# Performance work log

Measured on AMD Instinct MI355X. Metric: run time of the kernel, lower is better.

Reference implementation:

```python
import jax, jax.numpy as jnp
import numpy as np

HEADS = 5

def _conv2d(x, w, b=None, groups=1):
    y = jax.lax.conv_general_dilated(x, w, (1, 1), 'SAME', feature_group_count=groups,
                                     dimension_numbers=('NCHW', 'OIHW', 'NCHW'))
    return y if b is None else y + b[None, :, None, None]

def _conv1d(x, w):
    return jax.lax.conv_general_dilated(x, w, (1,), [(2, 2)], dimension_numbers=('NCH', 'OIH', 'NCH'))

def _bn(x, g, b, eps=1e-5):
    # torch BatchNorm2d in training mode: biased batch stats over (N,H,W)
    m = jnp.mean(x, (0, 2, 3), keepdims=True)
    v = jnp.var(x, (0, 2, 3), keepdims=True)
    return g[None, :, None, None] * (x - m) * jax.lax.rsqrt(v + eps) + b[None, :, None, None]

def _avg_pool3s2(x):
    # AvgPool2d(3, stride=2, padding=1), count_include_pad=True -> divide by 9
    s = jax.lax.reduce_window(x, 0.0, jax.lax.add, (1, 1, 3, 3), (1, 1, 2, 2),
                              [(0, 0), (0, 0), (1, 1), (1, 1)])
    return s / 9.0

def _max_pool2(x):
    return jax.lax.reduce_window(x, -jnp.inf, jax.lax.max, (1, 1, 2, 2), (1, 1, 2, 2), [(0, 0)] * 4)

def _gauss_kernel(ks, sigma, ch):
    # replicates cv2.getGaussianKernel(ks, sigma) outer-product, depthwise weight (ch,1,ks,ks)
    i = np.arange(ks, dtype=np.float64) - (ks - 1) / 2.0
    g = np.exp(-(i ** 2) / (2.0 * sigma ** 2))
    g = g / g.sum()
    k2 = np.outer(g, g).astype(np.float32)
    return jnp.asarray(np.broadcast_to(k2, (ch, 1, ks, ks)).copy())

def _forward(x, dwconv_w, dwconv_b, qkvl_w, qkvl_b, reproj_w, reproj_b, queries_w, queries_b,
             sff_low_w, sff_low_g, sff_low_b, sff_high_w, sff_high_g, sff_high_b,
             sff_c1_w, sff_c2_w, out_conv_w, out_bn_g, out_bn_b, out_proj_w, out_proj_b):
    n, C, h, w = x.shape
    C4 = C // 4
    shortcut = x
    # local branch: channel-split, depthwise conv / pointwise qkvl
    x1 = jax.nn.gelu(_conv2d(x[:, ::2], dwconv_w, dwconv_b, groups=C // 2), approximate=False)
    x2 = jax.nn.gelu(_conv2d(x[:, 1::2], qkvl_w, qkvl_b), approximate=False)
    x2 = x2.reshape(n, HEADS, C4, h, w)
    q = jnp.sum(x2[:, :-3], axis=1)              # (n, C4, h, w)
    k = x2[:, -3]
    q = _avg_pool3s2(q).reshape(n, C4, -1)       # h,w even -> same pooled size, pad branch dead
    k = _max_pool2(k).reshape(n, C4, -1)
    v = x2[:, -2].reshape(n, C4, h * w)
    lfeat = x2[:, -1]
    qk = jnp.einsum('ncp,ndp->ncd', q, k)        # (n, cq, ck)
    A = jax.nn.softmax(qk, axis=1)               # softmax over cq, transpose folded into einsum
    x2o = jnp.einsum('nqk,nqp->nkp', A, v).reshape(n, C4, h, w)
    eff = _conv2d(jnp.concatenate([x1, lfeat, x2o], axis=1), reproj_w, reproj_b)
    # global frequency (Laplacian pyramid) channel attention
    qx = _conv2d(x, queries_w, queries_b).reshape(n, -1, C)
    q_ = jnp.transpose(jax.nn.softmax(qx, axis=1), (0, 2, 1))    # (n, C, hw)
    sigma0, s = 1.6, 2.0 ** (1.0 / 3.0)
    G = shortcut
    pyr = [G]
    for i in range(3):
        G = _conv2d(G, _gauss_kernel(2 * i + 3, sigma0 * s ** i, C), groups=C)
        pyr.append(G)
    ctx = ((pyr[0] - pyr[1]) + (pyr[1] - pyr[2]) + (pyr[2] - pyr[3])).reshape(n, C, h * w)
    att = jnp.einsum('ncp,ndp->ncd', jax.nn.softmax(ctx, axis=2), ctx)   # (n, C, C)
    freq = x + jnp.einsum('nji,njp->nip', att, q_).reshape(n, C, h, w)   # att.T @ q_
    # SFF fusion
    x_low = jax.nn.relu(_bn(_conv2d(freq, sff_low_w), sff_low_g, sff_low_b))
    x_high = jax.nn.relu(_bn(_conv2d(eff, sff_high_w), sff_high_g, sff_high_b))
    pl = (jnp.mean(x_low ** 3.0, axis=(2, 3)) + 1e-12) ** (1.0 / 3.0)    # GeM p=3 -> (n, C)
    ph = (jnp.mean(x_high ** 3.0, axis=(2, 3)) + 1e-12) ** (1.0 / 3.0)
    d = jnp.stack([pl, ph], axis=2).reshape(n, 1, 2 * C)                 # interleave low/high per channel
    d = _conv1d(_conv1d(d, sff_c1_w), sff_c2_w)
    d = jax.nn.sigmoid(d.reshape(n, C, 2))
    f = d[:, :, 0][:, :, None, None] * x_low + d[:, :, 1][:, :, None, None] * x_high
    # BiSeNetOutput head (PixelShuffle(1) is identity)
    y = jax.nn.relu(_bn(_conv2d(f, out_conv_w), out_bn_g, out_bn_b))
    return _conv2d(y, out_proj_w, out_proj_b)

def _w(k, shape):
    fan_in = int(np.prod(shape[1:]))
    return jax.random.normal(k, shape, jnp.float32) / np.sqrt(fan_in)

def setup_inputs() -> dict:
    keys = jax.random.split(jax.random.key(0), 12)
    C = 128
    f32 = jnp.float32
    return {
        'x': jax.random.normal(keys[0], (8, C, 128, 128), f32),
        'dwconv_w': _w(keys[1], (C // 2, 1, 3, 3)), 'dwconv_b': jnp.zeros((C // 2,), f32),
        'qkvl_w': _w(keys[2], (C // 4 * HEADS, C // 2, 1, 1)), 'qkvl_b': jnp.zeros((C // 4 * HEADS,), f32),
        'reproj_w': _w(keys[3], (C, C, 1, 1)), 'reproj_b': jnp.zeros((C,), f32),
        'queries_w': _w(keys[4], (C, C, 1, 1)), 'queries_b': jnp.zeros((C,), f32),
        'sff_low_w': _w(keys[5], (C, C, 3, 3)), 'sff_low_g': jnp.ones((C,), f32), 'sff_low_b': jnp.zeros((C,), f32),
        'sff_high_w': _w(keys[6], (C, C, 3, 3)), 'sff_high_g': jnp.ones((C,), f32), 'sff_high_b': jnp.zeros((C,), f32),
        'sff_c1_w': _w(keys[7], (1, 1, 5)), 'sff_c2_w': _w(keys[8], (1, 1, 5)),
        'out_conv_w': _w(keys[9], (C, C, 3, 3)), 'out_bn_g': jnp.ones((C,), f32), 'out_bn_b': jnp.zeros((C,), f32),
        'out_proj_w': _w(keys[10], (C, C, 1, 1)), 'out_proj_b': jnp.zeros((C,), f32),
    }

def reference(x, dwconv_w, dwconv_b, qkvl_w, qkvl_b, reproj_w, reproj_b, queries_w, queries_b,
              sff_low_w, sff_low_g, sff_low_b, sff_high_w, sff_high_g, sff_high_b,
              sff_c1_w, sff_c2_w, out_conv_w, out_bn_g, out_bn_b, out_proj_w, out_proj_b):
    return _forward(x, dwconv_w, dwconv_b, qkvl_w, qkvl_b, reproj_w, reproj_b, queries_w, queries_b,
                    sff_low_w, sff_low_g, sff_low_b, sff_high_w, sff_high_g, sff_high_b,
                    sff_c1_w, sff_c2_w, out_conv_w, out_bn_g, out_bn_b, out_proj_w, out_proj_b)
```

## Files before the change

kernel.cpp:

```cpp
#include <hip/hip_runtime.h>
#include <hip/hip_bf16.h>
#include <cmath>

#define DEVFN __device__ __forceinline__

constexpr int HW = 16384;
constexpr long long U = 16777216LL;
constexpr long long NHWC_N = 2163200LL;

typedef __attribute__((ext_vector_type(8))) short bf16x8;
typedef __attribute__((ext_vector_type(4))) float f32x4;
typedef __attribute__((ext_vector_type(4))) unsigned short u16x4;

constexpr long long OFF_X1   = 0;
constexpr long long OFF_QS   = U/2;
constexpr long long OFF_KK   = 3*U/4;
constexpr long long OFF_X2O  = U/2;
constexpr long long OFF_V    = U;
constexpr long long OFF_LF   = U + U/4;
constexpr long long OFF_QP   = U + U/2;
constexpr long long OFF_KP   = U + U/2 + 1048576;
constexpr long long S0       = 2*U;
constexpr long long OFF_QKB  = S0;
constexpr long long OFF_AA   = S0 + 8192;
constexpr long long OFF_MQ   = S0 + 16384;
constexpr long long OFF_DQ   = S0 + 17408;
constexpr long long OFF_PMAX = S0 + 18432;
constexpr long long OFF_PSUM = S0 + 149504;
constexpr long long OFF_MC   = S0 + 280576;
constexpr long long OFF_DC   = S0 + 281600;
constexpr long long OFF_ATT  = S0 + 282624;
constexpr long long OFF_SSL  = S0 + 430080;
constexpr long long OFF_SSH  = S0 + 430336;
constexpr long long OFF_SSY  = S0 + 430592;
constexpr long long OFF_DV   = S0 + 430848;
constexpr long long OFF_D0   = S0 + 432896;
constexpr long long OFF_D1   = S0 + 433920;
constexpr long long OFF_WQK  = S0 + 434944;
constexpr long long OFF_WLOW  = OFF_PMAX;
constexpr long long OFF_WHIGH = OFF_PMAX + 73728;
constexpr long long OFF_WOUT  = OFF_PMAX + 147456;
constexpr long long DOFF_CTXP  = 9000000;
constexpr long long DOFF_PARTA = 9100000;
constexpr long long DOFF_PARTB = 9700000;

struct Taps { float g[7]; };

DEVFN float gelu_f(float v) { return 0.5f * v * (1.0f + erff(v * 0.7071067811865475f)); }
DEVFN unsigned short f2b(float f) {
  unsigned u = __float_as_uint(f);
  unsigned r = u + 0x7fffu + ((u >> 16) & 1u);
  return (unsigned short)(r >> 16);
}
DEVFN unsigned pk2(float a, float b) {
  return (unsigned)f2b(a) | ((unsigned)f2b(b) << 16);
}

__global__ __launch_bounds__(256) void k_dwconv(const float* __restrict__ x, const float* __restrict__ w9,
                                                const float* __restrict__ bia, float* __restrict__ out) {
  int g = blockIdx.x * 256 + threadIdx.x;
  int w = g & 127, h = (g >> 7) & 127, c = (g >> 14) & 63, n = g >> 20;
  const float* src = x + (long long)(n * 128 + 2 * c) * HW;
  float acc = bia[c];
  #pragma unroll
  for (int ky = 0; ky < 3; ++ky) {
    int h2 = h + ky - 1;
    if ((unsigned)h2 < 128u) {
      #pragma unroll
      for (int kx = 0; kx < 3; ++kx) {
        int w2 = w + kx - 1;
        if ((unsigned)w2 < 128u) acc = fmaf(w9[c * 9 + ky * 3 + kx], src[h2 * 128 + w2], acc);
      }
    }
  }
  out[(long long)(n * 64 + c) * HW + h * 128 + w] = gelu_f(acc);
}

__global__ __launch_bounds__(256) void k_wpackq(const float* __restrict__ w, unsigned short* __restrict__ wp) {
  int g = blockIdx.x * 256 + threadIdx.x;
  if (g < 10240) wp[g] = f2b(w[g]);
}

__global__ __launch_bounds__(256) void k_qkvlm(const float* __restrict__ x, const unsigned short* __restrict__ wqk,
                                               const float* __restrict__ bq, float* __restrict__ qs,
                                               float* __restrict__ kk, float* __restrict__ vv,
                                               float* __restrict__ lf) {
  __shared__ unsigned int Bs[64 * 36];
  const int t = threadIdx.x;
  const int bx = blockIdx.x, n = blockIdx.y;
  const int pxb = bx * 64;
  #pragma unroll
  for (int it = 0; it < 8; ++it) {
    int e = it * 256 + t;
    int px = e & 63, k2 = e >> 6;
    float v0 = x[(long long)(n * 128 + 4 * k2 + 1) * HW + pxb + px];
    float v1 = x[(long long)(n * 128 + 4 * k2 + 3) * HW + pxb + px];
    Bs[px * 36 + k2] = pk2(v0, v1);
  }
  __syncthreads();
  const int wid = t >> 6, lane = t & 63, l15 = lane & 15, l4 = lane >> 4;
  f32x4 acc[10];
  #pragma unroll
  for (int m = 0; m < 10; ++m) { f32x4 z = {0.f,0.f,0.f,0.f}; acc[m] = z; }
  #pragma unroll
  for (int ks = 0; ks < 2; ++ks) {
    bf16x8 bfr = *(const bf16x8*)(&Bs[(wid * 16 + l15) * 36 + ks * 16 + l4 * 4]);
    #pragma unroll
    for (int mf = 0; mf < 10; ++mf) {
      bf16x8 af = *(const bf16x8*)(wqk + (mf * 16 + l15) * 64 + ks * 32 + l4 * 8);
      acc[mf] = __builtin_amdgcn_mfma_f32_16x16x32_bf16(af, bfr, acc[mf], 0, 0, 0);
    }
  }
  float* sT = (float*)Bs;
  const int pxl = wid * 16 + l15;
  const int jo = t >> 3, p0 = (t & 7) * 8;
  #pragma unroll
  for (int tau = 0; tau < 4; ++tau) {
    __syncthreads();
    #pragma unroll
    for (int mf = 0; mf < 2; ++mf) {
      #pragma unroll
      for (int r = 0; r < 4; ++r) {
        int j = mf * 16 + l4 * 4 + r;
        float v;
        if (tau == 0)
          v = gelu_f(acc[mf][r] + bq[j]) + gelu_f(acc[mf + 2][r] + bq[32 + j]);
        else
          v = gelu_f(acc[2 + 2 * tau + mf][r] + bq[32 * (tau + 1) + j]);
        sT[j * 68 + pxl] = v;
      }
    }
    __syncthreads();
    float* dstp = (tau == 0) ? qs : (tau == 1) ? kk : (tau == 2) ? vv : lf;
    long long o = (long long)(n * 32 + jo) * HW + pxb + p0;
    #pragma unroll
    for (int q4 = 0; q4 < 2; ++q4)
      *(f32x4*)&dstp[o + q4 * 4] = *(const f32x4*)&sT[jo * 68 + p0 + q4 * 4];
  }
}

__global__ __launch_bounds__(256) void k_avgpool(const float* __restrict__ in, float* __restrict__ out) {
  int g = blockIdx.x * 256 + threadIdx.x;
  int ow = g & 63, oh = (g >> 6) & 63, c = (g >> 12) & 31, n = g >> 17;
  const float* src = in + (long long)(n * 32 + c) * HW;
  float s = 0.f;
  #pragma unroll
  for (int i = 0; i < 3; ++i) {
    int h = oh * 2 - 1 + i;
    if ((unsigned)h < 128u) {
      #pragma unroll
      for (int j = 0; j < 3; ++j) {
        int w = ow * 2 - 1 + j;
        if ((unsigned)w < 128u) s += src[h * 128 + w];
      }
    }
  }
  out[(long long)(n * 32 + c) * 4096 + oh * 64 + ow] = s * (1.f / 9.f);
}

__global__ __launch_bounds__(256) void k_maxpool(const float* __restrict__ in, float* __restrict__ out) {
  int g = blockIdx.x * 256 + threadIdx.x;
  int ow = g & 63, oh = (g >> 6) & 63, c = (g >> 12) & 31, n = g >> 17;
  const float* src = in + (long long)(n * 32 + c) * HW;
  float m = -3.0e38f;
  #pragma unroll
  for (int i = 0; i < 2; ++i)
    #pragma unroll
    for (int j = 0; j < 2; ++j)
      m = fmaxf(m, src[(oh * 2 + i) * 128 + ow * 2 + j]);
  out[(long long)(n * 32 + c) * 4096 + oh * 64 + ow] = m;
}

__global__ __launch_bounds__(256) void k_qk(const float* __restrict__ qp, const float* __restrict__ kp,
                                            float* __restrict__ qk) {
  int c = blockIdx.x, n = blockIdx.y;
  int t = threadIdx.x, d = t >> 3, r = t & 7;
  const float* qr = qp + (long long)(n * 32 + c) * 4096;
  const float* kr = kp + (long long)(n * 32 + d) * 4096;
  float acc = 0.f;
  for (int p = r; p < 4096; p += 8) acc = fmaf(qr[p], kr[p], acc);
  acc += __shfl_down(acc, 4, 8);
  acc += __shfl_down(acc, 2, 8);
  acc += __shfl_down(acc, 1, 8);
  if (r == 0) qk[(n * 32 + c) * 32 + d] = acc;
}

__global__ void k_qksm(const float* __restrict__ qk, float* __restrict__ A) {
  int n = blockIdx.x, d = threadIdx.x;
  float m = -3.0e38f;
  for (int c = 0; c < 32; ++c) m = fmaxf(m, qk[(n * 32 + c) * 32 + d]);
  float s = 0.f;
  for (int c = 0; c < 32; ++c) s += expf(qk[(n * 32 + c) * 32 + d] - m);
  float inv = 1.f / s;
  for (int c = 0; c < 32; ++c) A[(n * 32 + c) * 32 + d] = expf(qk[(n * 32 + c) * 32 + d] - m) * inv;
}

__global__ __launch_bounds__(256) void k_x2o(const float* __restrict__ A, const float* __restrict__ vsrc,
                                             float* __restrict__ out) {
  __shared__ float lA[1024];
  int t = threadIdx.x;
  int g = blockIdx.x * 256 + t;
  int n = g >> 14, p = g & 16383;
  for (int e = t; e < 1024; e += 256) lA[e] = A[n * 1024 + e];
  __syncthreads();
  float acc[32];
  #pragma unroll
  for (int i = 0; i < 32; ++i) acc[i] = 0.f;
  for (int q = 0; q < 32; ++q) {
    float vv = vsrc[(long long)(n * 32 + q) * HW + p];
    #pragma unroll
    for (int k2 = 0; k2 < 32; ++k2) acc[k2] = fmaf(lA[q * 32 + k2], vv, acc[k2]);
  }
  #pragma unroll
  for (int k2 = 0; k2 < 32; ++k2) out[(long long)(n * 32 + k2) * HW + p] = acc[k2];
}

enum { M_EFF = 0, M_QX = 1, M_OUT = 2, M_FREQ = 3 };

template <int MODE>
__global__ __launch_bounds__(256) void k_gemm1x1m(
    const float* __restrict__ Amat, const float* __restrict__ B0, const float* __restrict__ B1,
    const float* __restrict__ B2, const float* __restrict__ bias, const float* __restrict__ scale,
    const float* __restrict__ Mq, const float* __restrict__ invDq, const float* __restrict__ xres,
    void* __restrict__ outp) {
  __shared__ unsigned int As[128 * 36];
  __shared__ unsigned int Bs[128 * 36];
  const int t = threadIdx.x;
  const int bx = blockIdx.x, n = blockIdx.y;
  const int pxb = bx * 128;
  const int wid = t >> 6, lane = t & 63, l15 = lane & 15, l4 = lane >> 4;
  const int wy = wid >> 1, wx = wid & 1;
  f32x4 acc[4][4];
  #pragma unroll
  for (int i = 0; i < 4; ++i)
    #pragma unroll
    for (int j = 0; j < 4; ++j) { f32x4 z = {0.f,0.f,0.f,0.f}; acc[i][j] = z; }

  for (int kc = 0; kc < 2; ++kc) {
    __syncthreads();
    if (MODE == M_FREQ) {
      #pragma unroll
      for (int it = 0; it < 16; ++it) {
        int e = it * 256 + t;
        int i = e & 127, j2l = e >> 7;
        int j = kc * 64 + 2 * j2l;
        float v0 = Amat[(long long)(n * 128 + j) * 128 + i];
        float v1 = Amat[(long long)(n * 128 + j + 1) * 128 + i];
        As[i * 36 + j2l] = pk2(v0, v1);
      }
    } else {
      #pragma unroll
      for (int it = 0; it < 16; ++it) {
        int e = it * 256 + t;
        int m = e >> 5, k2l = e & 31;
        float2 v = *(const float2*)(&Amat[m * 128 + kc * 64 + 2 * k2l]);
        As[m * 36 + k2l] = pk2(v.x, v.y);
      }
    }
    if (MODE == M_FREQ) {
      #pragma unroll
      for (int it = 0; it < 16; ++it) {
        int e = it * 256 + t;
        int j2l = e & 31, px = e >> 5;
        int j = kc * 64 + 2 * j2l;
        long long qb = ((long long)n * HW + pxb + px) * 128 + j;
        float2 v = *(const float2*)(&B0[qb]);
        float e0 = expf(v.x - Mq[n * 128 + j]) * invDq[n * 128 + j];
        float e1 = expf(v.y - Mq[n * 128 + j + 1]) * invDq[n * 128 + j + 1];
        Bs[px * 36 + j2l] = pk2(e0, e1);
      }
    } else {
      #pragma unroll
      for (int it = 0; it < 16; ++it) {
        int e = it * 256 + t;
        int px = e & 127, k2l = e >> 7;
        int ci = kc * 64 + 2 * k2l;
        float v0, v1;
        if (MODE == M_EFF) {
          if (ci < 64) {
            v0 = B0[(long long)(n * 64 + ci) * HW + pxb + px];
            v1 = B0[(long long)(n * 64 + ci + 1) * HW + pxb + px];
          } else if (ci < 96) {
            v0 = B1[(long long)(n * 32 + ci - 64) * HW + pxb + px];
            v1 = B1[(long long)(n * 32 + ci - 63) * HW + pxb + px];
          } else {
            v0 = B2[(long long)(n * 32 + ci - 96) * HW + pxb + px];
            v1 = B2[(long long)(n * 32 + ci - 95) * HW + pxb + px];
          }
        } else if (MODE == M_QX) {
          v0 = B0[(long long)(n * 128 + ci) * HW + pxb + px];
          v1 = B0[(long long)(n * 128 + ci + 1) * HW + pxb + px];
        } else {
          float u0 = B0[(long long)(n * 128 + ci) * HW + pxb + px];
          float u1 = B0[(long long)(n * 128 + ci + 1) * HW + pxb + px];
          v0 = fmaxf(fmaf(u0, scale[ci], scale[128 + ci]), 0.f);
          v1 = fmaxf(fmaf(u1, scale[ci + 1], scale[128 + ci + 1]), 0.f);
        }
        Bs[px * 36 + k2l] = pk2(v0, v1);
      }
    }
    __syncthreads();
    #pragma unroll
    for (int ks = 0; ks < 2; ++ks) {
      bf16x8 af[4], bfr[4];
      #pragma unroll
      for (int mf = 0; mf < 4; ++mf)
        af[mf] = *(const bf16x8*)(&As[(wy * 64 + mf * 16 + l15) * 36 + ks * 16 + l4 * 4]);
      #pragma unroll
      for (int nf = 0; nf < 4; ++nf)
        bfr[nf] = *(const bf16x8*)(&Bs[(wx * 64 + nf * 16 + l15) * 36 + ks * 16 + l4 * 4]);
      #pragma unroll
      for (int mf = 0; mf < 4; ++mf)
        #pragma unroll
        for (int nf = 0; nf < 4; ++nf)
          acc[mf][nf] = __builtin_amdgcn_mfma_f32_16x16x32_bf16(af[mf], bfr[nf], acc[mf][nf], 0, 0, 0);
    }
  }
  if (MODE == M_EFF || MODE == M_FREQ) {
    unsigned short* oT = (unsigned short*)outp;
    #pragma unroll
    for (int nf = 0; nf < 4; ++nf) {
      int px = pxb + wx * 64 + nf * 16 + l15;
      int hh = px >> 7, wwp = (px & 127) + 1;
      long long rb = (long long)n * NHWC_N + ((long long)(hh + 1) * 130 + wwp) * 128;
      #pragma unroll
      for (int mf = 0; mf < 4; ++mf) {
        int ch = wy * 64 + mf * 16 + l4 * 4;
        u16x4 pk;
        #pragma unroll
        for (int r = 0; r < 4; ++r) {
          float v = acc[mf][nf][r] + ((MODE == M_EFF) ? bias[ch + r] : 0.f);
          if (MODE == M_FREQ) v += xres[(long long)(n * 128 + ch + r) * HW + px];
          pk[r] = f2b(v);
        }
        *(u16x4*)(&oT[rb + ch]) = pk;
      }
    }
  } else {
    float* of = (float*)outp;
    #pragma unroll
    for (int mf = 0; mf < 4; ++mf)
      #pragma unroll
      for (int nf = 0; nf < 4; ++nf) {
        int px = pxb + wx * 64 + nf * 16 + l15;
        #pragma unroll
        for (int r = 0; r < 4; ++r) {
          int ch = wy * 64 + mf * 16 + l4 * 4 + r;
          of[(long long)(n * 128 + ch) * HW + px] = acc[mf][nf][r] + bias[ch];
        }
      }
  }
}

__global__ __launch_bounds__(128) void k_qx_stat1(const float* __restrict__ qx, float* __restrict__ pm,
                                                  float* __restrict__ ps) {
  int c = blockIdx.x, n = blockIdx.y, w = threadIdx.x;
  long long base = (long long)(n * 128 + c) * HW + w;
  float m = -3.0e38f;
  for (int h = 0; h < 128; ++h) m = fmaxf(m, qx[base + h * 128]);
  float s = 0.f;
  for (int h = 0; h < 128; ++h) s += expf(qx[base + h * 128] - m);
  pm[(n * 128 + c) * 128 + w] = m;
  ps[(n * 128 + c) * 128 + w] = s;
}
__global__ __launch_bounds__(128) void k_qx_stat2(const float* __restrict__ pm, const float* __restrict__ ps,
                                                  float* __restrict__ Mq, float* __restrict__ Dq) {
  int n = blockIdx.x, w = threadIdx.x;
  float M = -3.0e38f;
  for (int c = 0; c < 128; ++c) M = fmaxf(M, pm[(n * 128 + c) * 128 + w]);
  float D = 0.f;
  for (int c = 0; c < 128; ++c) D += ps[(n * 128 + c) * 128 + w] * expf(pm[(n * 128 + c) * 128 + w] - M);
  Mq[n * 128 + w] = M;
  Dq[n * 128 + w] = 1.f / D;
}

constexpr int BROWS = 44;
constexpr int BSTR  = 144;

template <int R, int HLO, int HHI, int VLO, int VHI>
DEVFN void blur_stage4(float* sA, float* sB, const float* __restrict__ g, int h0, int t) {
  __syncthreads();
  constexpr int HN = (HHI - HLO + 1) * 32;
  for (int e = t; e < HN; e += 256) {
    int r = HLO + (e >> 5), g4 = e & 31;
    int base = r * BSTR + 8 + g4 * 4;
    f32x4 a = *(const f32x4*)&sA[base - 4];
    f32x4 b = *(const f32x4*)&sA[base];
    f32x4 c = *(const f32x4*)&sA[base + 4];
    float m[12] = {a[0], a[1], a[2], a[3], b[0], b[1], b[2], b[3], c[0], c[1], c[2], c[3]};
    f32x4 s;
    #pragma unroll
    for (int j = 0; j < 4; ++j) {
      float acc = 0.f;
      #pragma unroll
      for (int d = -R; d <= R; ++d) acc = fmaf(g[d + R], m[4 + j + d], acc);
      s[j] = acc;
    }
    *(f32x4*)&sB[base] = s;
  }
  __syncthreads();
  constexpr int VN = (VHI - VLO + 1) * 32;
  for (int e = t; e < VN; e += 256) {
    int r = VLO + (e >> 5), g4 = e & 31;
    int base = r * BSTR + 8 + g4 * 4;
    f32x4 s = {0.f, 0.f, 0.f, 0.f};
    #pragma unroll
    for (int d = -R; d <= R; ++d) {
      f32x4 v = *(const f32x4*)&sB[base + d * BSTR];
      #pragma unroll
      for (int j = 0; j < 4; ++j) s[j] = fmaf(g[d + R], v[j], s[j]);
    }
    int h = h0 - 6 + r;
    if ((unsigned)h >= 128u) { f32x4 z = {0.f, 0.f, 0.f, 0.f}; s = z; }
    *(f32x4*)&sA[base] = s;
  }
}

__global__ __launch_bounds__(256) void k_blur3(const float* __restrict__ x, float* __restrict__ ctx,
                                               float* __restrict__ ctxp, Taps t3, Taps t5, Taps t7) {
  __shared__ float sA[BROWS * BSTR];
  __shared__ float sB[BROWS * BSTR];
  __shared__ float rm[256], rs[256];
  const int t = threadIdx.x;
  const int ht = blockIdx.x, h0 = ht * 32;
  const long long nc = blockIdx.y;
  const float* src = x + nc * HW;
  for (int e = t; e < BROWS * BSTR; e += 256) {
    int r = e / BSTR, wp = e % BSTR;
    int w = wp - 8, h = h0 - 6 + r;
    sA[e] = ((unsigned)h < 128u && (unsigned)w < 128u) ? src[h * 128 + w] : 0.f;
  }
  blur_stage4<1, 0, 43, 1, 42>(sA, sB, t3.g, h0, t);
  blur_stage4<2, 1, 42, 3, 40>(sA, sB, t5.g, h0, t);
  blur_stage4<3, 3, 40, 6, 37>(sA, sB, t7.g, h0, t);
  __syncthreads();
  long long ob = nc * HW + (long long)h0 * 128;
  float lm = -3.0e38f, lsum = 0.f;
  for (int e = t; e < 1024; e += 256) {
    int r = e >> 5, g4 = e & 31;
    f32x4 xs = *(const f32x4*)&src[(h0 + r) * 128 + g4 * 4];
    f32x4 bl = *(const f32x4*)&sA[(6 + r) * BSTR + 8 + g4 * 4];
    f32x4 v;
    #pragma unroll
    for (int j = 0; j < 4; ++j) {
      v[j] = xs[j] - bl[j];
      float val = v[j];
      if (val > lm) { lsum = lsum * expf(lm - val) + 1.f; lm = val; }
      else lsum += expf(val - lm);
    }
    *(f32x4*)&ctx[ob + r * 128 + g4 * 4] = v;
  }
  rm[t] = lm; rs[t] = lsum; __syncthreads();
  for (int o = 128; o > 0; o >>= 1) {
    if (t < o) {
      float m2 = rm[t + o], s2 = rs[t + o];
      float M = fmaxf(rm[t], m2);
      rs[t] = rs[t] * expf(rm[t] - M) + s2 * expf(m2 - M);
      rm[t] = M;
    }
    __syncthreads();
  }
  if (t == 0) { ctxp[nc * 8 + ht * 2] = rm[0]; ctxp[nc * 8 + ht * 2 + 1] = rs[0]; }
}

__global__ __launch_bounds__(256) void k_ctx_red(const float* __restrict__ ctxp, float* __restrict__ Mc,
                                                 float* __restrict__ Dc) {
  int g = blockIdx.x * 256 + threadIdx.x;
  float M = -3.0e38f, S = 0.f;
  #pragma unroll
  for (int i = 0; i < 4; ++i) {
    float m2 = ctxp[g * 8 + i * 2], s2 = ctxp[g * 8 + i * 2 + 1];
    float Mn = fmaxf(M, m2);
    S = S * expf(M - Mn) + s2 * expf(m2 - Mn);
    M = Mn;
  }
  Mc[g] = M; Dc[g] = 1.f / S;
}

__global__ __launch_bounds__(256) void k_attm(const float* __restrict__ ctx, const float* __restrict__ Mc,
                                              const float* __restrict__ invDc, float* __restrict__ attp) {
  __shared__ unsigned int As[128 * 36];
  __shared__ unsigned int Bs[128 * 36];
  const int t = threadIdx.x, sp = blockIdx.x, n = blockIdx.y;
  const int wid = t >> 6, lane = t & 63, l15 = lane & 15, l4 = lane >> 4;
  const int wy = wid >> 1, wx = wid & 1;
  f32x4 acc[4][4];
  #pragma unroll
  for (int i = 0; i < 4; ++i)
    #pragma unroll
    for (int j = 0; j < 4; ++j) { f32x4 z = {0.f,0.f,0.f,0.f}; acc[i][j] = z; }
  for (int kc = 0; kc < 8; ++kc) {
    __syncthreads();
    int pb = sp * 512 + kc * 64;
    #pragma unroll
    for (int it = 0; it < 16; ++it) {
      int e = it * 256 + t;
      int row = e >> 5, p2 = e & 31;
      float2 v = *(const float2*)(&ctx[(long long)(n * 128 + row) * HW + pb + 2 * p2]);
      float m = Mc[n * 128 + row], d = invDc[n * 128 + row];
      Bs[row * 36 + p2] = pk2(v.x, v.y);
      As[row * 36 + p2] = pk2(expf(v.x - m) * d, expf(v.y - m) * d);
    }
    __syncthreads();
    #pragma unroll
    for (int ks = 0; ks < 2; ++ks) {
      bf16x8 af[4], bfr[4];
      #pragma unroll
      for (int mf = 0; mf < 4; ++mf)
        af[mf] = *(const bf16x8*)(&As[(wy * 64 + mf * 16 + l15) * 36 + ks * 16 + l4 * 4]);
      #pragma unroll
      for (int nf = 0; nf < 4; ++nf)
        bfr[nf] = *(const bf16x8*)(&Bs[(wx * 64 + nf * 16 + l15) * 36 + ks * 16 + l4 * 4]);
      #pragma unroll
      for (int mf = 0; mf < 4; ++mf)
        #pragma unroll
        for (int nf = 0; nf < 4; ++nf)
          acc[mf][nf] = __builtin_amdgcn_mfma_f32_16x16x32_bf16(af[mf], bfr[nf], acc[mf][nf], 0, 0, 0);
    }
  }
  long long ob = (long long)(sp * 8 + n) * 16384;
  #pragma unroll
  for (int mf = 0; mf < 4; ++mf)
    #pragma unroll
    for (int nf = 0; nf < 4; ++nf) {
      int d = wx * 64 + nf * 16 + l15;
      #pragma unroll
      for (int r = 0; r < 4; ++r) {
        int c = wy * 64 + mf * 16 + l4 * 4 + r;
        attp[ob + c * 128 + d] = acc[mf][nf][r];
      }
    }
}

__global__ __launch_bounds__(256) void k_attred(const float* __restrict__ attp, float* __restrict__ att) {
  int g = blockIdx.x * 256 + threadIdx.x;
  float s = 0.f;
  for (int sp = 0; sp < 32; ++sp) s += attp[(long long)sp * 131072 + g];
  att[g] = s;
}

__global__ __launch_bounds__(256) void k_wpack(const float* __restrict__ w, unsigned short* __restrict__ wp) {
  int g = blockIdx.x * 256 + threadIdx.x;
  int ci = g & 127;
  int tap = (g >> 7) % 9;
  int co = g / 1152;
  wp[g] = f2b(w[co * 1152 + ci * 9 + tap]);
}

__global__ __launch_bounds__(256) void k_haloz(unsigned short* __restrict__ p) {
  int idx = blockIdx.x * 256 + threadIdx.x;
  if (idx >= 66048) return;
  int n = idx / 8256;
  int r = idx % 8256;
  int cell = r >> 4, q = r & 15;
  int h, w;
  if (cell < 130)      { h = 0;   w = cell; }
  else if (cell < 260) { h = 129; w = cell - 130; }
  else if (cell < 388) { h = cell - 260 + 1; w = 0; }
  else                 { h = cell - 388 + 1; w = 129; }
  uint4 z = {0u, 0u, 0u, 0u};
  *(uint4*)(p + (long long)n * NHWC_N + ((long long)h * 130 + w) * 128 + q * 8) = z;
}

__global__ __launch_bounds__(256) void k_conv3l(const unsigned short* __restrict__ inT,
                                                const unsigned short* __restrict__ wp,
                                                float* __restrict__ out,
                                                float* __restrict__ part) {
  __shared__ unsigned short Bs[2 * 12480];
  const int t = threadIdx.x;
  const int h0 = blockIdx.x, n = blockIdx.y;
  const int wid = t >> 6, lane = t & 63;
  const int wy = wid >> 1, wx = wid & 1;
  const int l15 = lane & 15, l4 = lane >> 4;
  f32x4 acc[4][4];
  #pragma unroll
  for (int i = 0; i < 4; ++i)
    #pragma unroll
    for (int j = 0; j < 4; ++j) { f32x4 z = {0.f, 0.f, 0.f, 0.f}; acc[i][j] = z; }
  const unsigned short* abase = wp + (wy * 64 + l15) * 1152 + l4 * 8;

  auto STAGE = [&](int kc, int buf) {
    const unsigned short* gb = inT + (long long)n * NHWC_N + kc * 32;
    #pragma unroll
    for (int it = 0; it < 7; ++it) {
      int cbase = it * 256 + wid * 64;
      int c = cbase + lane;
      if (c < 1560) {
        int row = c / 520, rem = c % 520;
        int w = rem >> 2, slot = rem & 3;
        int sg = slot ^ ((w >> 1) & 3);
        const unsigned short* src = gb + ((long long)(h0 + row) * 130 + w) * 128 + sg * 8;
        __builtin_amdgcn_global_load_lds(
            (const __attribute__((address_space(1))) unsigned int*)src,
            (__attribute__((address_space(3))) unsigned int*)&Bs[buf * 12480 + cbase * 8],
            16, 0, 0);
      }
    }
  };

  STAGE(0, 0);
  #pragma unroll
  for (int kc = 0; kc < 4; ++kc) {
    __syncthreads();
    if (kc < 3) STAGE(kc + 1, (kc + 1) & 1);
    const int lb = (kc & 1) * 12480;
    #pragma unroll
    for (int ky = 0; ky < 3; ++ky) {
      #pragma unroll
      for (int kx = 0; kx < 3; ++kx) {
        const int tap = ky * 3 + kx;
        bf16x8 af[4], bfr[4];
        #pragma unroll
        for (int cf = 0; cf < 4; ++cf)
          af[cf] = *(const bf16x8*)(abase + cf * 16 * 1152 + tap * 128 + kc * 32);
        #pragma unroll
        for (int pf = 0; pf < 4; ++pf) {
          int w = wx * 64 + pf * 16 + l15 + kx;
          int sr = l4 ^ ((w >> 1) & 3);
          bfr[pf] = *(const bf16x8*)(&Bs[lb + ky * 4160 + w * 32 + sr * 8]);
        }
        #pragma unroll
        for (int cf = 0; cf < 4; ++cf)
          #pragma unroll
          for (int pf = 0; pf < 4; ++pf)
            acc[cf][pf] = __builtin_amdgcn_mfma_f32_16x16x32_bf16(af[cf], bfr[pf], acc[cf][pf], 0, 0, 0);
      }
    }
  }
  long long ob = (long long)n * 128 * HW + h0 * 128;
  #pragma unroll
  for (int cf = 0; cf < 4; ++cf)
    #pragma unroll
    for (int pf = 0; pf < 4; ++pf) {
      int co = wy * 64 + cf * 16 + l4 * 4;
      int w  = wx * 64 + pf * 16 + l15;
      #pragma unroll
      for (int r = 0; r < 4; ++r)
        out[ob + (long long)(co + r) * HW + w] = acc[cf][pf][r];
    }
  __shared__ float redS[4][64], redQ[4][64];
  #pragma unroll
  for (int cf = 0; cf < 4; ++cf)
    #pragma unroll
    for (int r = 0; r < 4; ++r) {
      float s = 0.f, q = 0.f;
      #pragma unroll
      for (int pf = 0; pf < 4; ++pf) { float v = acc[cf][pf][r]; s += v; q = fmaf(v, v, q); }
      #pragma unroll
      for (int off = 1; off < 16; off <<= 1) { s += __shfl_xor(s, off, 16); q += __shfl_xor(q, off, 16); }
      if (l15 == 0) { redS[wid][cf * 16 + l4 * 4 + r] = s; redQ[wid][cf * 16 + l4 * 4 + r] = q; }
    }
  __syncthreads();
  if (t < 128) {
    int wy2 = t >> 6, col = t & 63;
    int co = wy2 * 64 + col;
    float s = redS[wy2 * 2][col] + redS[wy2 * 2 + 1][col];
    float q = redQ[wy2 * 2][col] + redQ[wy2 * 2 + 1][col];
    long long pb = ((long long)(n * 128 + h0) * 128 + co) * 2;
    part[pb] = s; part[pb + 1] = q;
  }
}

__global__ __launch_bounds__(256) void k_bnred(const float* __restrict__ part, const float* __restrict__ g,
                                               const float* __restrict__ bb, float* __restrict__ ssout) {
  int c = blockIdx.x, t = threadIdx.x;
  float s = 0.f, q = 0.f;
  for (int b = t; b < 1024; b += 256) {
    s += part[((long long)b * 128 + c) * 2];
    q += part[((long long)b * 128 + c) * 2 + 1];
  }
  __shared__ float r1[256], r2[256];
  r1[t] = s; r2[t] = q; __syncthreads();
  for (int o = 128; o > 0; o >>= 1) { if (t < o) { r1[t] += r1[t + o]; r2[t] += r2[t + o]; } __syncthreads(); }
  if (t == 0) {
    float mean = r1[0] / 131072.f;
    float var = r2[0] / 131072.f - mean * mean;
    float sc = g[c] * rsqrtf(var + 1e-5f);
    ssout[c] = sc;
    ssout[128 + c] = bb[c] - mean * sc;
  }
}

__global__ __launch_bounds__(256) void k_power(const float* __restrict__ in, const float* __restrict__ ss,
                                               float* __restrict__ dst, int off) {
  int c = blockIdx.x, n = blockIdx.y, t = threadIdx.x;
  float sc = ss[c], sh = ss[128 + c];
  long long base = (long long)(n * 128 + c) * HW;
  float s = 0.f;
  for (int i = t; i < HW; i += 256) {
    float r = fmaxf(fmaf(in[base + i], sc, sh), 0.f);
    s += r * r * r;
  }
  __shared__ float red[256];
  red[t] = s; __syncthreads();
  for (int o = 128; o > 0; o >>= 1) { if (t < o) red[t] += red[t + o]; __syncthreads(); }
  if (t == 0) dst[n * 256 + 2 * c + off] = cbrtf(red[0] * (1.f / 16384.f) + 1e-12f);
}

__global__ __launch_bounds__(256) void k_dvec(const float* __restrict__ din, const float* __restrict__ c1,
                                              const float* __restrict__ c2, float* __restrict__ d0,
                                              float* __restrict__ d1) {
  __shared__ float a[256], b[256];
  int n = blockIdx.x, t = threadIdx.x;
  a[t] = din[n * 256 + t];
  __syncthreads();
  float acc = 0.f;
  #pragma unroll
  for (int k = 0; k < 5; ++k) { int j = t + k - 2; if (0 <= j && j < 256) acc = fmaf(c1[k], a[j], acc); }
  b[t] = acc; __syncthreads();
  float acc2 = 0.f;
  #pragma unroll
  for (int k = 0; k < 5; ++k) { int j = t + k - 2; if (0 <= j && j < 256) acc2 = fmaf(c2[k], b[j], acc2); }
  float sg = 1.f / (1.f + expf(-acc2));
  if ((t & 1) == 0) d0[n * 128 + (t >> 1)] = sg; else d1[n * 128 + (t >> 1)] = sg;
}

__global__ __launch_bounds__(256) void k_fmixT(const float* __restrict__ low, const float* __restrict__ high,
                                               const float* __restrict__ ssl, const float* __restrict__ ssh,
                                               const float* __restrict__ d0, const float* __restrict__ d1,
                                               unsigned short* __restrict__ outT) {
  __shared__ float ld[64 * 129];
  int t = threadIdx.x;
  int h = blockIdx.x, n = blockIdx.y;
  const long long sb = (long long)n * 128 * HW + h * 128;
  unsigned short* dst = outT + (long long)n * NHWC_N + ((long long)(h + 1) * 130 + 1) * 128;
  for (int half = 0; half < 2; ++half) {
    __syncthreads();
    for (int e = t; e < 8192; e += 256) {
      int c = e >> 7, w = e & 127;
      int cg = half * 64 + c;
      float xl = fmaxf(fmaf(low[sb + (long long)cg * HW + w], ssl[cg], ssl[128 + cg]), 0.f);
      float xh = fmaxf(fmaf(high[sb + (long long)cg * HW + w], ssh[cg], ssh[128 + cg]), 0.f);
      ld[c * 129 + w] = d0[n * 128 + cg] * xl + d1[n * 128 + cg] * xh;
    }
    __syncthreads();
    for (int q = t; q < 1024; q += 256) {
      int w = q >> 3, cg8 = q & 7;
      bf16x8 pk;
      #pragma unroll
      for (int u = 0; u < 8; ++u) pk[u] = (short)f2b(ld[(cg8 * 8 + u) * 129 + w]);
      *(bf16x8*)(dst + (long long)w * 128 + half * 64 + cg8 * 8) = pk;
    }
  }
}

static void make_taps(int ks, double sigma, Taps* tp) {
  double c = (ks - 1) / 2.0, sum = 0.0, v[7];
  for (int i = 0; i < ks; ++i) { double d = i - c; v[i] = std::exp(-d * d / (2.0 * sigma * sigma)); sum += v[i]; }
  for (int i = 0; i < 7; ++i) tp->g[i] = (i < ks) ? (float)(v[i] / sum) : 0.f;
}

extern "C" void kernel_launch(void* const* d_in, const int* in_sizes, int n_in,
                              void* d_out, int out_size, void* d_ws, size_t ws_size,
                              hipStream_t stream) {
  const float* x         = (const float*)d_in[0];
  const float* dwconv_w  = (const float*)d_in[1];
  const float* dwconv_b  = (const float*)d_in[2];
  const float* qkvl_w    = (const float*)d_in[3];
  const float* qkvl_b    = (const float*)d_in[4];
  const float* reproj_w  = (const float*)d_in[5];
  const float* reproj_b  = (const float*)d_in[6];
  const float* queries_w = (const float*)d_in[7];
  const float* queries_b = (const float*)d_in[8];
  const float* sff_low_w = (const float*)d_in[9];
  const float* sff_low_g = (const float*)d_in[10];
  const float* sff_low_b = (const float*)d_in[11];
  const float* sff_high_w= (const float*)d_in[12];
  const float* sff_high_g= (const float*)d_in[13];
  const float* sff_high_b= (const float*)d_in[14];
  const float* sff_c1_w  = (const float*)d_in[15];
  const float* sff_c2_w  = (const float*)d_in[16];
  const float* out_conv_w= (const float*)d_in[17];
  const float* out_bn_g  = (const float*)d_in[18];
  const float* out_bn_b  = (const float*)d_in[19];
  const float* out_proj_w= (const float*)d_in[20];
  const float* out_proj_b= (const float*)d_in[21];
  float* ws  = (float*)d_ws;
  float* out = (float*)d_out;

  float* x1   = ws + OFF_X1;
  float* qs   = ws + OFF_QS;
  float* kk   = ws + OFF_KK;
  float* x2o  = ws + OFF_X2O;
  float* vv   = ws + OFF_V;
  float* lf   = ws + OFF_LF;
  float* qp   = ws + OFF_QP;
  float* kp   = ws + OFF_KP;
  float* ctx  = ws + U;
  float* attp = ws;
  float* qx   = ws;
  float* lowc = ws;
  float* highc= ws + U;
  float* ybuf = ws;
  float* qkb  = ws + OFF_QKB;
  float* Abuf = ws + OFF_AA;
  float* Mq   = ws + OFF_MQ;
  float* Dq   = ws + OFF_DQ;
  float* pm   = ws + OFF_PMAX;
  float* psv  = ws + OFF_PSUM;
  float* Mc   = ws + OFF_MC;
  float* Dc   = ws + OFF_DC;
  float* att  = ws + OFF_ATT;
  float* ssl  = ws + OFF_SSL;
  float* ssh  = ws + OFF_SSH;
  float* ssy  = ws + OFF_SSY;
  float* dv   = ws + OFF_DV;
  float* d0v  = ws + OFF_D0;
  float* d1v  = ws + OFF_D1;
  unsigned short* wqk   = (unsigned short*)(ws + OFF_WQK);
  unsigned short* wlow  = (unsigned short*)(ws + OFF_WLOW);
  unsigned short* whigh = (unsigned short*)(ws + OFF_WHIGH);
  unsigned short* wout  = (unsigned short*)(ws + OFF_WOUT);
  unsigned short* effT  = (unsigned short*)out;
  unsigned short* freqT = (unsigned short*)(ws + U);
  unsigned short* fT    = (unsigned short*)out;
  float* ctxp  = out + DOFF_CTXP;
  float* partA = out + DOFF_PARTA;
  float* partB = out + DOFF_PARTB;

  Taps t3, t5, t7;
  const double s3 = std::pow(2.0, 1.0 / 3.0);
  make_taps(3, 1.6, &t3);
  make_taps(5, 1.6 * s3, &t5);
  make_taps(7, 1.6 * s3 * s3, &t7);

  dim3 b256(256), b128(128);

  k_wpackq<<<dim3(40), b256, 0, stream>>>(qkvl_w, wqk);
  k_haloz<<<dim3(258), b256, 0, stream>>>(effT);
  k_dwconv<<<dim3(32768), b256, 0, stream>>>(x, dwconv_w, dwconv_b, x1);
  k_qkvlm<<<dim3(256, 8), b256, 0, stream>>>(x, wqk, qkvl_b, qs, kk, vv, lf);
  k_avgpool<<<dim3(4096), b256, 0, stream>>>(qs, qp);
  k_maxpool<<<dim3(4096), b256, 0, stream>>>(kk, kp);
  k_qk<<<dim3(32, 8), b256, 0, stream>>>(qp, kp, qkb);
  k_qksm<<<dim3(8), dim3(32), 0, stream>>>(qkb, Abuf);
  k_x2o<<<dim3(512), b256, 0, stream>>>(Abuf, vv, x2o);
  k_gemm1x1m<M_EFF><<<dim3(128, 8), b256, 0, stream>>>(reproj_w, x1, lf, x2o, reproj_b,
                                                       nullptr, nullptr, nullptr, nullptr, effT);
  k_blur3<<<dim3(4, 1024), b256, 0, stream>>>(x, ctx, ctxp, t3, t5, t7);
  k_ctx_red<<<dim3(4), b256, 0, stream>>>(ctxp, Mc, Dc);
  k_attm<<<dim3(32, 8), b256, 0, stream>>>(ctx, Mc, Dc, attp);
  k_attred<<<dim3(512), b256, 0, stream>>>(attp, att);
  k_gemm1x1m<M_QX><<<dim3(128, 8), b256, 0, stream>>>(queries_w, x, nullptr, nullptr, queries_b,
                                                      nullptr, nullptr, nullptr, nullptr, qx);
  k_qx_stat1<<<dim3(128, 8), b128, 0, stream>>>(qx, pm, psv);
  k_qx_stat2<<<dim3(8), b128, 0, stream>>>(pm, psv, Mq, Dq);
  k_wpack<<<dim3(576), b256, 0, stream>>>(sff_low_w, wlow);
  k_wpack<<<dim3(576), b256, 0, stream>>>(sff_high_w, whigh);
  k_wpack<<<dim3(576), b256, 0, stream>>>(out_conv_w, wout);
  k_haloz<<<dim3(258), b256, 0, stream>>>(freqT);
  k_gemm1x1m<M_FREQ><<<dim3(128, 8), b256, 0, stream>>>(att, qx, nullptr, nullptr, nullptr,
                                                        nullptr, Mq, Dq, x, freqT);
  k_conv3l<<<dim3(128, 8), b256, 0, stream>>>(freqT, wlow, lowc, partA);
  k_conv3l<<<dim3(128, 8), b256, 0, stream>>>(effT, whigh, highc, partB);
  k_bnred<<<dim3(128), b256, 0, stream>>>(partA, sff_low_g, sff_low_b, ssl);
  k_bnred<<<dim3(128), b256, 0, stream>>>(partB, sff_high_g, sff_high_b, ssh);
  k_power<<<dim3(128, 8), b256, 0, stream>>>(lowc, ssl, dv, 0);
  k_power<<<dim3(128, 8), b256, 0, stream>>>(highc, ssh, dv, 1);
  k_dvec<<<dim3(8), b256, 0, stream>>>(dv, sff_c1_w, sff_c2_w, d0v, d1v);
  k_fmixT<<<dim3(128, 8), b256, 0, stream>>>(lowc, highc, ssl, ssh, d0v, d1v, fT);
  k_conv3l<<<dim3(128, 8), b256, 0, stream>>>(fT, wout, ybuf, partA);
  k_bnred<<<dim3(128), b256, 0, stream>>>(partA, out_bn_g, out_bn_b, ssy);
  k_gemm1x1m<M_OUT><<<dim3(128, 8), b256, 0, stream>>>(out_proj_w, ybuf, nullptr, nullptr, out_proj_b,
                                                       ssy, nullptr, nullptr, nullptr, out);
  (void)in_sizes; (void)n_in; (void)out_size; (void)ws_size;
}
```

Baseline: 1.037 ms.

## Compute two output rows per block in 3x3 conv to reuse weights and halo rows

Each conv3l block now produces two output rows instead of one. It stages four input rows into LDS instead of three and reuses each weight fragment for both rows. This cuts global weight loads per output and redundant halo-row staging, but doubles the accumulator registers to 128 floats per lane. The grid is halved to 512 blocks, which lowers occupancy and parallelism. The BN partial reduction is resized to match.

```diff
diff --git a/kernel.cpp b/kernel.cpp
--- a/kernel.cpp
+++ b/kernel.cpp
@@ -566,33 +566,36 @@
                                                 const unsigned short* __restrict__ wp,
                                                 float* __restrict__ out,
                                                 float* __restrict__ part) {
-  __shared__ unsigned short Bs[2 * 12480];
+  __shared__ unsigned short Bs[2 * 16640];
   const int t = threadIdx.x;
-  const int h0 = blockIdx.x, n = blockIdx.y;
+  const int bx = blockIdx.x, n = blockIdx.y;
+  const int h0 = bx * 2;
   const int wid = t >> 6, lane = t & 63;
   const int wy = wid >> 1, wx = wid & 1;
   const int l15 = lane & 15, l4 = lane >> 4;
-  f32x4 acc[4][4];
+  f32x4 acc[4][4][2];
   #pragma unroll
   for (int i = 0; i < 4; ++i)
     #pragma unroll
-    for (int j = 0; j < 4; ++j) { f32x4 z = {0.f, 0.f, 0.f, 0.f}; acc[i][j] = z; }
+    for (int j = 0; j < 4; ++j)
+      #pragma unroll
+      for (int ro = 0; ro < 2; ++ro) { f32x4 z = {0.f, 0.f, 0.f, 0.f}; acc[i][j][ro] = z; }
   const unsigned short* abase = wp + (wy * 64 + l15) * 1152 + l4 * 8;
 
   auto STAGE = [&](int kc, int buf) {
     const unsigned short* gb = inT + (long long)n * NHWC_N + kc * 32;
     #pragma unroll
-    for (int it = 0; it < 7; ++it) {
+    for (int it = 0; it < 9; ++it) {
       int cbase = it * 256 + wid * 64;
       int c = cbase + lane;
-      if (c < 1560) {
+      if (c < 2080) {
         int row = c / 520, rem = c % 520;
         int w = rem >> 2, slot = rem & 3;
         int sg = slot ^ ((w >> 1) & 3);
         const unsigned short* src = gb + ((long long)(h0 + row) * 130 + w) * 128 + sg * 8;
         __builtin_amdgcn_global_load_lds(
             (const __attribute__((address_space(1))) unsigned int*)src,
-            (__attribute__((address_space(3))) unsigned int*)&Bs[buf * 12480 + cbase * 8],
+            (__attribute__((address_space(3))) unsigned int*)&Bs[buf * 16640 + cbase * 8],
             16, 0, 0);
       }
     }
@@ -603,13 +606,13 @@
   for (int kc = 0; kc < 4; ++kc) {
     __syncthreads();
     if (kc < 3) STAGE(kc + 1, (kc + 1) & 1);
-    const int lb = (kc & 1) * 12480;
+    const int lb = (kc & 1) * 16640;
     #pragma unroll
     for (int ky = 0; ky < 3; ++ky) {
       #pragma unroll
       for (int kx = 0; kx < 3; ++kx) {
         const int tap = ky * 3 + kx;
-        bf16x8 af[4], bfr[4];
+        bf16x8 af[4], bfr[4][2];
         #pragma unroll
         for (int cf = 0; cf < 4; ++cf)
           af[cf] = *(const bf16x8*)(abase + cf * 16 * 1152 + tap * 128 + kc * 32);
@@ -617,27 +620,34 @@
         for (int pf = 0; pf < 4; ++pf) {
           int w = wx * 64 + pf * 16 + l15 + kx;
           int sr = l4 ^ ((w >> 1) & 3);
-          bfr[pf] = *(const bf16x8*)(&Bs[lb + ky * 4160 + w * 32 + sr * 8]);
+          #pragma unroll
+          for (int ro = 0; ro < 2; ++ro)
+            bfr[pf][ro] = *(const bf16x8*)(&Bs[lb + (ro + ky) * 4160 + w * 32 + sr * 8]);
         }
         #pragma unroll
         for (int cf = 0; cf < 4; ++cf)
           #pragma unroll
           for (int pf = 0; pf < 4; ++pf)
-            acc[cf][pf] = __builtin_amdgcn_mfma_f32_16x16x32_bf16(af[cf], bfr[pf], acc[cf][pf], 0, 0, 0);
-      }
-    }
-  }
-  long long ob = (long long)n * 128 * HW + h0 * 128;
-  #pragma unroll
-  for (int cf = 0; cf < 4; ++cf)
-    #pragma unroll
-    for (int pf = 0; pf < 4; ++pf) {
-      int co = wy * 64 + cf * 16 + l4 * 4;
-      int w  = wx * 64 + pf * 16 + l15;
-      #pragma unroll
-      for (int r = 0; r < 4; ++r)
-        out[ob + (long long)(co + r) * HW + w] = acc[cf][pf][r];
-    }
+            #pragma unroll
+            for (int ro = 0; ro < 2; ++ro)
+              acc[cf][pf][ro] = __builtin_amdgcn_mfma_f32_16x16x32_bf16(af[cf], bfr[pf][ro], acc[cf][pf][ro], 0, 0, 0);
+      }
+    }
+  }
+  #pragma unroll
+  for (int ro = 0; ro < 2; ++ro) {
+    long long ob = (long long)n * 128 * HW + (h0 + ro) * 128;
+    #pragma unroll
+    for (int cf = 0; cf < 4; ++cf)
+      #pragma unroll
+      for (int pf = 0; pf < 4; ++pf) {
+        int co = wy * 64 + cf * 16 + l4 * 4;
+        int w  = wx * 64 + pf * 16 + l15;
+        #pragma unroll
+        for (int r = 0; r < 4; ++r)
+          out[ob + (long long)(co + r) * HW + w] = acc[cf][pf][ro][r];
+      }
+  }
   __shared__ float redS[4][64], redQ[4][64];
   #pragma unroll
   for (int cf = 0; cf < 4; ++cf)
@@ -645,7 +655,9 @@
     for (int r = 0; r < 4; ++r) {
       float s = 0.f, q = 0.f;
       #pragma unroll
-      for (int pf = 0; pf < 4; ++pf) { float v = acc[cf][pf][r]; s += v; q = fmaf(v, v, q); }
+      for (int pf = 0; pf < 4; ++pf)
+        #pragma unroll
+        for (int ro = 0; ro < 2; ++ro) { float v = acc[cf][pf][ro][r]; s += v; q = fmaf(v, v, q); }
       #pragma unroll
       for (int off = 1; off < 16; off <<= 1) { s += __shfl_xor(s, off, 16); q += __shfl_xor(q, off, 16); }
       if (l15 == 0) { redS[wid][cf * 16 + l4 * 4 + r] = s; redQ[wid][cf * 16 + l4 * 4 + r] = q; }
@@ -656,7 +668,7 @@
     int co = wy2 * 64 + col;
     float s = redS[wy2 * 2][col] + redS[wy2 * 2 + 1][col];
     float q = redQ[wy2 * 2][col] + redQ[wy2 * 2 + 1][col];
-    long long pb = ((long long)(n * 128 + h0) * 128 + co) * 2;
+    long long pb = ((long long)(n * 64 + bx) * 128 + co) * 2;
     part[pb] = s; part[pb + 1] = q;
   }
 }
@@ -665,7 +677,7 @@
                                                const float* __restrict__ bb, float* __restrict__ ssout) {
   int c = blockIdx.x, t = threadIdx.x;
   float s = 0.f, q = 0.f;
-  for (int b = t; b < 1024; b += 256) {
+  for (int b = t; b < 512; b += 256) {
     s += part[((long long)b * 128 + c) * 2];
     q += part[((long long)b * 128 + c) * 2 + 1];
   }
@@ -851,15 +863,15 @@
   k_haloz<<<dim3(258), b256, 0, stream>>>(freqT);
   k_gemm1x1m<M_FREQ><<<dim3(128, 8), b256, 0, stream>>>(att, qx, nullptr, nullptr, nullptr,
                                                         nullptr, Mq, Dq, x, freqT);
-  k_conv3l<<<dim3(128, 8), b256, 0, stream>>>(freqT, wlow, lowc, partA);
-  k_conv3l<<<dim3(128, 8), b256, 0, stream>>>(effT, whigh, highc, partB);
+  k_conv3l<<<dim3(64, 8), b256, 0, stream>>>(freqT, wlow, lowc, partA);
+  k_conv3l<<<dim3(64, 8), b256, 0, stream>>>(effT, whigh, highc, partB);
   k_bnred<<<dim3(128), b256, 0, stream>>>(partA, sff_low_g, sff_low_b, ssl);
   k_bnred<<<dim3(128), b256, 0, stream>>>(partB, sff_high_g, sff_high_b, ssh);
   k_power<<<dim3(128, 8), b256, 0, stream>>>(lowc, ssl, dv, 0);
   k_power<<<dim3(128, 8), b256, 0, stream>>>(highc, ssh, dv, 1);
   k_dvec<<<dim3(8), b256, 0, stream>>>(dv, sff_c1_w, sff_c2_w, d0v, d1v);
   k_fmixT<<<dim3(128, 8), b256, 0, stream>>>(lowc, highc, ssl, ssh, d0v, d1v, fT);
-  k_conv3l<<<dim3(128, 8), b256, 0, stream>>>(fT, wout, ybuf, partA);
+  k_conv3l<<<dim3(64, 8), b256, 0, stream>>>(fT, wout, ybuf, partA);
   k_bnred<<<dim3(128), b256, 0, stream>>>(partA, out_bn_g, out_bn_b, ssy);
   k_gemm1x1m<M_OUT><<<dim3(128, 8), b256, 0, stream>>>(out_proj_w, ybuf, nullptr, nullptr, out_proj_b,
                                                        ssy, nullptr, nullptr, nullptr, out);
```

Measured after the change: 1.025 ms (median of 2 runs). About the same (-1.1%).
